# Optimization experiments

Measured on AMD Instinct MI355X. Metric: run time of the kernel, lower is better.

## Reference

```python
import jax, jax.numpy as jnp
import numpy as np

B, N, DIM = 16, 4096, 256
EXP = 4
COV_EPS = 1e-08


def setup_inputs() -> dict:
    key = jax.random.key(0)
    ks = jax.random.split(key, 9)
    s = 1.0 / np.sqrt(DIM)
    sh = 1.0 / np.sqrt(DIM * EXP)
    return {
        "x": jax.random.normal(ks[0], (B, N, DIM), dtype=jnp.float32),
        # IsoFFN: Linear(dim, 4*dim) -> GELU -> Linear(4*dim, dim) + residual (dropout inactive at eval)
        "W1": jax.random.uniform(ks[1], (DIM, DIM * EXP), minval=-s, maxval=s, dtype=jnp.float32),
        "b1": jnp.zeros((DIM * EXP,), jnp.float32),
        "W2": jax.random.uniform(ks[2], (DIM * EXP, DIM), minval=-sh, maxval=sh, dtype=jnp.float32),
        "b2": jnp.zeros((DIM,), jnp.float32),
        # eigenvalue head: Linear(dim, 3) + Softplus
        "Wval": jax.random.uniform(ks[3], (DIM, 3), minval=-s, maxval=s, dtype=jnp.float32),
        "bval": jnp.zeros((3,), jnp.float32),
        # eigenvector head: Linear(dim, 9)
        "Wvec": jax.random.uniform(ks[4], (DIM, 9), minval=-s, maxval=s, dtype=jnp.float32),
        "bvec": jnp.zeros((9,), jnp.float32),
    }


def reference(x, W1, b1, W2, b2, Wval, bval, Wvec, bvec):
    b, n, c = x.shape
    # IsoFFN (eval mode: dropout = identity), residual connection
    h = x + jax.nn.gelu(x @ W1 + b1) @ W2 + b2
    # eigenvalue head -> positive eigenvalues -> diagonal [B*N, 3, 3]
    eigvals = jax.nn.softplus(h @ Wval + bval).reshape(b * n, 3)
    L = jnp.zeros((b * n, 3, 3), h.dtype).at[:, jnp.arange(3), jnp.arange(3)].set(eigvals)
    # eigenvector head -> batched tiny QR to orthonormalize
    V = (h @ Wvec + bvec).reshape(b * n, 3, 3)
    Q, _ = jnp.linalg.qr(V)  # batched 3x3 QR
    # cov = Q L Q^T
    cov = jnp.einsum('bij,bjk,blk->bil', Q, L, Q).reshape(b, n, 3, 3)
    cov = (cov + jnp.swapaxes(cov, -2, -1)) * 0.5
    cov = cov + COV_EPS * jnp.eye(3, dtype=cov.dtype)
    return cov
```

## Files before the change

### kernel.cpp

```cpp
#include <hip/hip_runtime.h>
#include <cstdint>
#include <cstddef>

#define TOKENS   65536
#define KDIM     256
#define HIDDEN   1024
#define BM       128
#define HC       32
#define NCHUNK   32
#define NTHREADS 512
#define NBLOCKS  (TOKENS / BM)

#define GOFF  131072
#define B1OFF 147456
#define LDS_BYTES 151552

using f16x8 = __attribute__((ext_vector_type(8))) _Float16;
using f16x4 = __attribute__((ext_vector_type(4))) _Float16;
using f32x4 = __attribute__((ext_vector_type(4))) float;
using u32x4 = __attribute__((ext_vector_type(4))) uint32_t;

__device__ __align__(16) _Float16 g_W1h[NCHUNK * HC * KDIM];
__device__ __align__(16) _Float16 g_W1l[NCHUNK * HC * KDIM];
__device__ __align__(16) _Float16 g_W2h[NCHUNK * KDIM * HC];
__device__ __align__(16) _Float16 g_W2l[NCHUNK * KDIM * HC];
__device__ __align__(16) _Float16 g_Whh[16 * KDIM];
__device__ __align__(16) _Float16 g_Whl[16 * KDIM];

__global__ __launch_bounds__(256) void prep_kernel(
    const float* __restrict__ W1, const float* __restrict__ W2,
    const float* __restrict__ Wval, const float* __restrict__ Wvec) {
  const int tid = blockIdx.x * 256 + threadIdx.x;
  if (tid < 32768) {
    const int c = tid >> 10, n = (tid >> 5) & 31, gd = tid & 31;
    const int g = gd ^ (n & 7);
    const int hid = c * 32 + n;
    f16x8 hv, lv;
#pragma unroll
    for (int j = 0; j < 8; ++j) {
      const float wv = W1[(g * 8 + j) * HIDDEN + hid];
      const _Float16 hi = (_Float16)wv;
      hv[j] = hi;
      lv[j] = (_Float16)(wv - (float)hi);
    }
    const int dst = c * 8192 + n * 256 + gd * 8;
    *(f16x8*)(g_W1h + dst) = hv;
    *(f16x8*)(g_W1l + dst) = lv;
  } else if (tid < 65536) {
    const int t = tid - 32768;
    const int c = t >> 10, n = (t >> 2) & 255, gd = t & 3;
    const int g = gd ^ ((n >> 1) & 3);
    f16x8 hv, lv;
#pragma unroll
    for (int j = 0; j < 8; ++j) {
      const float wv = W2[(c * 32 + g * 8 + j) * KDIM + n];
      const _Float16 hi = (_Float16)wv;
      hv[j] = hi;
      lv[j] = (_Float16)(wv - (float)hi);
    }
    const int dst = c * 8192 + n * 32 + gd * 8;
    *(f16x8*)(g_W2h + dst) = hv;
    *(f16x8*)(g_W2l + dst) = lv;
  } else if (tid < 65536 + 4096) {
    const int e = tid - 65536;
    const int j16 = e >> 8, k = e & 255;
    float wv = 0.f;
    if (j16 < 3) wv = Wval[k * 3 + j16];
    else if (j16 < 12) wv = Wvec[k * 9 + (j16 - 3)];
    const _Float16 hi = (_Float16)wv;
    g_Whh[e] = hi;
    g_Whl[e] = (_Float16)(wv - (float)hi);
  }
}

__device__ __forceinline__ void stage_chunk(char* buf, int c, int w, int lane) {
  const int plane = w >> 1, half = w & 1;
  const _Float16* g;
  if      (plane == 0) g = g_W1h;
  else if (plane == 1) g = g_W1l;
  else if (plane == 2) g = g_W2h;
  else                 g = g_W2l;
  const char* s = (const char*)g + (size_t)c * 16384 + half * 8192 + lane * 16;
  char* d = buf + plane * 16384 + half * 8192;
#pragma unroll
  for (int i = 0; i < 8; ++i) {
    __builtin_amdgcn_global_load_lds(
        (__attribute__((address_space(1))) void*)(void*)(s + i * 1024),
        (__attribute__((address_space(3))) void*)(d + i * 1024), 16, 0, 0);
  }
}

__device__ __forceinline__ f16x8 unpack_half(const u32x4 a, const u32x4 b, uint32_t sel) {
  u32x4 r;
  r[0] = __builtin_amdgcn_perm(a[1], a[0], sel);
  r[1] = __builtin_amdgcn_perm(a[3], a[2], sel);
  r[2] = __builtin_amdgcn_perm(b[1], b[0], sel);
  r[3] = __builtin_amdgcn_perm(b[3], b[2], sel);
  return __builtin_bit_cast(f16x8, r);
}

__global__ __launch_bounds__(NTHREADS, 2) void fused_kernel(
    const float* __restrict__ x, const float* __restrict__ b1,
    const float* __restrict__ b2, const float* __restrict__ bval,
    const float* __restrict__ bvec, float* __restrict__ out) {
  extern __shared__ char smem[];
  const int tid  = threadIdx.x;
  const int lane = tid & 63;
  const int w    = tid >> 6;
  const int wm   = w >> 1;
  const int wn   = w & 1;
  const int l15  = lane & 15;
  const int lg   = lane >> 4;
  const int64_t R = (int64_t)blockIdx.x * BM;

  {
    float* b1l = (float*)(smem + B1OFF);
    b1l[tid]       = b1[tid];
    b1l[tid + 512] = b1[tid + 512];
  }

  {
    const float* xg = x + R * KDIM;
#pragma unroll
    for (int i = 0; i < 16; ++i) {
      const int fidx = tid + NTHREADS * i;
      const int row  = fidx >> 6;
      const int f4   = fidx & 63;
      const float4 v = *(const float4*)(xg + row * KDIM + f4 * 4);
      const _Float16 h0 = (_Float16)v.x, h1 = (_Float16)v.y,
                     h2 = (_Float16)v.z, h3 = (_Float16)v.w;
      f16x4 hv = {h0, h1, h2, h3};
      f16x4 lv = {(_Float16)(v.x - (float)h0), (_Float16)(v.y - (float)h1),
                  (_Float16)(v.z - (float)h2), (_Float16)(v.w - (float)h3)};
      const uint32_t off = (uint32_t)(row * 512) +
                           (((uint32_t)(f4 * 8)) ^ ((row & 7) << 4));
      *(f16x4*)(smem + off)         = hv;
      *(f16x4*)(smem + 65536 + off) = lv;
    }
  }
  __syncthreads();

  f16x8 xah[2][8], xal[2][8];
#pragma unroll
  for (int mt = 0; mt < 2; ++mt) {
    const int row = wm * 32 + mt * 16 + l15;
    const uint32_t rbase = row * 512;
    const uint32_t swz = (row & 7) << 4;
#pragma unroll
    for (int ks = 0; ks < 8; ++ks) {
      const uint32_t off = rbase + (((uint32_t)((ks * 32 + lg * 8) * 2)) ^ swz);
      xah[mt][ks] = *(const f16x8*)(smem + off);
      xal[mt][ks] = *(const f16x8*)(smem + 65536 + off);
    }
  }
  asm volatile("s_waitcnt lgkmcnt(0)" ::: "memory");
  __builtin_amdgcn_s_barrier();
  __builtin_amdgcn_sched_barrier(0);

  stage_chunk(smem,         0, w, lane);
  stage_chunk(smem + 65536, 1, w, lane);

  const f32x4 z4 = {0.f, 0.f, 0.f, 0.f};
  f32x4 acc2[2][8];
#pragma unroll
  for (int mt = 0; mt < 2; ++mt)
#pragma unroll
    for (int nt = 0; nt < 8; ++nt) acc2[mt][nt] = z4;

#pragma unroll 1
  for (int t = 0; t < NCHUNK; ++t) {
    char* buf = smem + ((t & 1) ? 65536 : 0);
    if (t == NCHUNK - 1) { asm volatile("s_waitcnt vmcnt(0)" ::: "memory"); }
    else                 { asm volatile("s_waitcnt vmcnt(8)" ::: "memory"); }
    __builtin_amdgcn_s_barrier();
    __builtin_amdgcn_sched_barrier(0);

    f32x4 accA[2] = {z4, z4}, accB[2] = {z4, z4}, accC[2] = {z4, z4};
    {
      const int n = wn * 16 + l15;
      const uint32_t nbase = (uint32_t)(n * 512);
      const uint32_t nswz  = (uint32_t)((n & 7) << 4);
#pragma unroll
      for (int ks = 0; ks < 8; ++ks) {
        const uint32_t off = nbase + (((uint32_t)(ks * 64 + lg * 16)) ^ nswz);
        const f16x8 bh = *(const f16x8*)(buf + off);
        const f16x8 bl = *(const f16x8*)(buf + 16384 + off);
#pragma unroll
        for (int mt = 0; mt < 2; ++mt) {
          accA[mt] = __builtin_amdgcn_mfma_f32_16x16x32_f16(xah[mt][ks], bh, accA[mt], 0, 0, 0);
          accB[mt] = __builtin_amdgcn_mfma_f32_16x16x32_f16(xah[mt][ks], bl, accB[mt], 0, 0, 0);
          accC[mt] = __builtin_amdgcn_mfma_f32_16x16x32_f16(xal[mt][ks], bh, accC[mt], 0, 0, 0);
        }
      }
    }

    {
      const float bv = ((const float*)(smem + B1OFF))[t * 32 + wn * 16 + l15];
      const int gcol = wn * 16 + l15;
#pragma unroll
      for (int mt = 0; mt < 2; ++mt) {
#pragma unroll
        for (int r = 0; r < 4; ++r) {
          const float v  = accA[mt][r] + accB[mt][r] + accC[mt][r] + bv;
          const float u  = 0.79788456080286535588f * (v + 0.044715f * v * v * v);
          const float e  = __expf(2.f * u);
          const float th = 1.f - 2.f / (e + 1.f);
          const float gv = 0.5f * v * (1.f + th);
          const _Float16 gh = (_Float16)gv;
          const _Float16 gl = (_Float16)(gv - (float)gh);
          const uint32_t pk = (uint32_t)__builtin_bit_cast(unsigned short, gh) |
                              ((uint32_t)__builtin_bit_cast(unsigned short, gl) << 16);
          const int grow = wm * 32 + mt * 16 + lg * 4 + r;
          const uint32_t off = (uint32_t)(GOFF + grow * 128) +
                               (((uint32_t)(gcol * 4)) ^ ((grow & 7) << 4));
          *(uint32_t*)(smem + off) = pk;
        }
      }
    }
    asm volatile("s_waitcnt lgkmcnt(0)" ::: "memory");
    __builtin_amdgcn_s_barrier();
    __builtin_amdgcn_sched_barrier(0);

    {
      f16x8 ah[2], al[2];
#pragma unroll
      for (int mt = 0; mt < 2; ++mt) {
        const int row = wm * 32 + mt * 16 + l15;
        const uint32_t sw = (uint32_t)((row & 7) << 4);
        const uint32_t base = (uint32_t)(GOFF + row * 128);
        const u32x4 w0 = *(const u32x4*)(smem + base + (((uint32_t)(lg * 32)) ^ sw));
        const u32x4 w1 = *(const u32x4*)(smem + base + (((uint32_t)(lg * 32 + 16)) ^ sw));
        ah[mt] = unpack_half(w0, w1, 0x05040100u);
        al[mt] = unpack_half(w0, w1, 0x07060302u);
      }
#pragma unroll
      for (int nt = 0; nt < 8; ++nt) {
        const int n = wn * 128 + nt * 16 + l15;
        const uint32_t off = (uint32_t)(n * 64) +
                             (((uint32_t)(lg * 16)) ^ (((n >> 1) & 3) << 4));
        const f16x8 bh = *(const f16x8*)(buf + 32768 + off);
        const f16x8 bl = *(const f16x8*)(buf + 49152 + off);
#pragma unroll
        for (int mt = 0; mt < 2; ++mt) {
          acc2[mt][nt] = __builtin_amdgcn_mfma_f32_16x16x32_f16(ah[mt], bh, acc2[mt][nt], 0, 0, 0);
          acc2[mt][nt] = __builtin_amdgcn_mfma_f32_16x16x32_f16(ah[mt], bl, acc2[mt][nt], 0, 0, 0);
          acc2[mt][nt] = __builtin_amdgcn_mfma_f32_16x16x32_f16(al[mt], bh, acc2[mt][nt], 0, 0, 0);
        }
      }
    }
    __builtin_amdgcn_sched_barrier(0);
    __builtin_amdgcn_s_barrier();
    __builtin_amdgcn_sched_barrier(0);
    if (t + 2 < NCHUNK) stage_chunk(buf, t + 2, w, lane);
  }

  {
    const float* xg = x + R * KDIM;
#pragma unroll
    for (int nt = 0; nt < 8; ++nt) {
      const float bv = b2[wn * 128 + nt * 16 + l15];
#pragma unroll
      for (int mt = 0; mt < 2; ++mt) {
#pragma unroll
        for (int r = 0; r < 4; ++r) {
          const int row = wm * 32 + mt * 16 + lg * 4 + r;
          const int col = wn * 128 + nt * 16 + l15;
          const float h = acc2[mt][nt][r] + xg[row * KDIM + col] + bv;
          acc2[mt][nt][r] = h;
          const uint32_t off = (uint32_t)(row * 512) +
                               (((uint32_t)(col * 2)) ^ ((row & 7) << 4));
          *(_Float16*)(smem + off) = (_Float16)h;
        }
      }
    }
  }
  __syncthreads();

  f32x4 hacc = z4;
  const int hrow = wm * 32 + wn * 16 + l15;
  const uint32_t hbase = hrow * 512;
  const uint32_t hswz  = (hrow & 7) << 4;
#pragma unroll
  for (int ks = 0; ks < 8; ++ks) {
    const uint32_t off = hbase + (((uint32_t)((ks * 32 + lg * 8) * 2)) ^ hswz);
    const f16x8 af  = *(const f16x8*)(smem + off);
    const f16x8 bhf = *(const f16x8*)(g_Whh + l15 * 256 + ks * 32 + lg * 8);
    const f16x8 blf = *(const f16x8*)(g_Whl + l15 * 256 + ks * 32 + lg * 8);
    hacc = __builtin_amdgcn_mfma_f32_16x16x32_f16(af, bhf, hacc, 0, 0, 0);
    hacc = __builtin_amdgcn_mfma_f32_16x16x32_f16(af, blf, hacc, 0, 0, 0);
  }
  __syncthreads();

#pragma unroll
  for (int nt = 0; nt < 8; ++nt) {
#pragma unroll
    for (int mt = 0; mt < 2; ++mt) {
#pragma unroll
      for (int r = 0; r < 4; ++r) {
        const int row = wm * 32 + mt * 16 + lg * 4 + r;
        const int col = wn * 128 + nt * 16 + l15;
        const float h = acc2[mt][nt][r];
        const _Float16 hh = (_Float16)h;
        const uint32_t off = (uint32_t)(row * 512) +
                             (((uint32_t)(col * 2)) ^ ((row & 7) << 4));
        *(_Float16*)(smem + off) = (_Float16)(h - (float)hh);
      }
    }
  }
  __syncthreads();

#pragma unroll
  for (int ks = 0; ks < 8; ++ks) {
    const uint32_t off = hbase + (((uint32_t)((ks * 32 + lg * 8) * 2)) ^ hswz);
    const f16x8 af  = *(const f16x8*)(smem + off);
    const f16x8 bhf = *(const f16x8*)(g_Whh + l15 * 256 + ks * 32 + lg * 8);
    hacc = __builtin_amdgcn_mfma_f32_16x16x32_f16(af, bhf, hacc, 0, 0, 0);
  }
  const float hb = (l15 < 3) ? bval[l15] : ((l15 < 12) ? bvec[l15 - 3] : 0.f);
#pragma unroll
  for (int r = 0; r < 4; ++r) hacc[r] += hb;

  float* hstg = (float*)(smem + 65536);
#pragma unroll
  for (int r = 0; r < 4; ++r) {
    const int row = wm * 32 + wn * 16 + lg * 4 + r;
    hstg[row * 16 + l15] = hacc[r];
  }
  if (lane < 16) {
    const int row = wm * 32 + wn * 16 + lane;
    const float* hs = hstg + row * 16;
    float sp[3];
#pragma unroll
    for (int i = 0; i < 3; ++i) {
      const float s = hs[i];
      sp[i] = fmaxf(s, 0.f) + log1pf(__expf(-fabsf(s)));
    }
    const float a0 = hs[3], a1 = hs[6], a2 = hs[9];
    const float b0 = hs[4], bc1 = hs[7], bc2 = hs[10];
    const float na = a0 * a0 + a1 * a1 + a2 * a2;
    const float ia = 1.f / sqrtf(fmaxf(na, 1e-30f));
    const float q00 = a0 * ia, q01 = a1 * ia, q02 = a2 * ia;
    const float d  = q00 * b0 + q01 * bc1 + q02 * bc2;
    const float u0 = b0 - d * q00, u1 = bc1 - d * q01, u2 = bc2 - d * q02;
    const float nu = u0 * u0 + u1 * u1 + u2 * u2;
    const float iu = 1.f / sqrtf(fmaxf(nu, 1e-30f));
    const float q10 = u0 * iu, q11 = u1 * iu, q12 = u2 * iu;
    const float q20 = q01 * q12 - q02 * q11;
    const float q21 = q02 * q10 - q00 * q12;
    const float q22 = q00 * q11 - q01 * q10;
    const float c00 = sp[0]*q00*q00 + sp[1]*q10*q10 + sp[2]*q20*q20 + 1e-8f;
    const float c11 = sp[0]*q01*q01 + sp[1]*q11*q11 + sp[2]*q21*q21 + 1e-8f;
    const float c22 = sp[0]*q02*q02 + sp[1]*q12*q12 + sp[2]*q22*q22 + 1e-8f;
    const float c01 = sp[0]*q00*q01 + sp[1]*q10*q11 + sp[2]*q20*q21;
    const float c02 = sp[0]*q00*q02 + sp[1]*q10*q12 + sp[2]*q20*q22;
    const float c12 = sp[0]*q01*q02 + sp[1]*q11*q12 + sp[2]*q21*q22;
    float* o = out + (size_t)(R + row) * 9;
    o[0] = c00; o[1] = c01; o[2] = c02;
    o[3] = c01; o[4] = c11; o[5] = c12;
    o[6] = c02; o[7] = c12; o[8] = c22;
  }
}

extern "C" void kernel_launch(void* const* d_in, const int* in_sizes, int n_in,
                              void* d_out, int out_size, void* d_ws, size_t ws_size,
                              hipStream_t stream) {
  const float* x    = (const float*)d_in[0];
  const float* W1   = (const float*)d_in[1];
  const float* b1   = (const float*)d_in[2];
  const float* W2   = (const float*)d_in[3];
  const float* b2   = (const float*)d_in[4];
  const float* Wval = (const float*)d_in[5];
  const float* bval = (const float*)d_in[6];
  const float* Wvec = (const float*)d_in[7];
  const float* bvec = (const float*)d_in[8];
  float* out = (float*)d_out;
  (void)in_sizes; (void)n_in; (void)out_size; (void)d_ws; (void)ws_size;

  hipFuncSetAttribute((const void*)fused_kernel,
                      hipFuncAttributeMaxDynamicSharedMemorySize, LDS_BYTES);

  prep_kernel<<<272, 256, 0, stream>>>(W1, W2, Wval, Wvec);
  fused_kernel<<<NBLOCKS, NTHREADS, LDS_BYTES, stream>>>(x, b1, b2, bval, bvec, out);
}
```

Baseline: 287.6 us.

## Software-pipeline GEMM1 and GEMM2 across chunks with double-buffered GELU tiles

Restructures the chunk loop so GEMM1 for chunk T runs in the same phase as GEMM2 for chunk T-1, using double-buffered G tiles and separate W1/W2 staging buffers. This cuts the number of barriers per chunk from three to two and lets the MFMA work from both GEMMs interleave. It also merges two correction accumulators into one, simplifies the GELU into a single exp and fast divide, and loads b1 from global memory one chunk ahead instead of staging it in LDS. LDS use grows to 160KB, and the changed staging order and barrier scheme could introduce hazards.

Result: slower. 384.1 us (+33.6%).

```diff
diff --git a/kernel.cpp b/kernel.cpp
--- a/kernel.cpp
+++ b/kernel.cpp
@@ -11,9 +11,9 @@
 #define NTHREADS 512
 #define NBLOCKS  (TOKENS / BM)
 
+#define W2OFF 65536
 #define GOFF  131072
-#define B1OFF 147456
-#define LDS_BYTES 151552
+#define LDS_BYTES 163840
 
 using f16x8 = __attribute__((ext_vector_type(8))) _Float16;
 using f16x4 = __attribute__((ext_vector_type(4))) _Float16;
@@ -73,17 +73,23 @@
   }
 }
 
-__device__ __forceinline__ void stage_chunk(char* buf, int c, int w, int lane) {
-  const int plane = w >> 1, half = w & 1;
-  const _Float16* g;
-  if      (plane == 0) g = g_W1h;
-  else if (plane == 1) g = g_W1l;
-  else if (plane == 2) g = g_W2h;
-  else                 g = g_W2l;
-  const char* s = (const char*)g + (size_t)c * 16384 + half * 8192 + lane * 16;
-  char* d = buf + plane * 16384 + half * 8192;
-#pragma unroll
-  for (int i = 0; i < 8; ++i) {
+__device__ __forceinline__ void stage_W1(char* smem, int par, int c, int w, int lane) {
+  const char* base = (w < 4) ? (const char*)g_W1h : (const char*)g_W1l;
+  const char* s = base + (size_t)c * 16384 + (size_t)(w & 3) * 4096 + (size_t)lane * 16;
+  char* d = smem + par * 32768 + ((w < 4) ? 0 : 16384) + (w & 3) * 4096;
+#pragma unroll
+  for (int i = 0; i < 4; ++i) {
+    __builtin_amdgcn_global_load_lds(
+        (__attribute__((address_space(1))) void*)(void*)(s + i * 1024),
+        (__attribute__((address_space(3))) void*)(d + i * 1024), 16, 0, 0);
+  }
+}
+__device__ __forceinline__ void stage_W2(char* smem, int par, int c, int w, int lane) {
+  const char* base = (w < 4) ? (const char*)g_W2h : (const char*)g_W2l;
+  const char* s = base + (size_t)c * 16384 + (size_t)(w & 3) * 4096 + (size_t)lane * 16;
+  char* d = smem + W2OFF + par * 32768 + ((w < 4) ? 0 : 16384) + (w & 3) * 4096;
+#pragma unroll
+  for (int i = 0; i < 4; ++i) {
     __builtin_amdgcn_global_load_lds(
         (__attribute__((address_space(1))) void*)(void*)(s + i * 1024),
         (__attribute__((address_space(3))) void*)(d + i * 1024), 16, 0, 0);
@@ -97,6 +103,114 @@
   r[2] = __builtin_amdgcn_perm(b[1], b[0], sel);
   r[3] = __builtin_amdgcn_perm(b[3], b[2], sel);
   return __builtin_bit_cast(f16x8, r);
+}
+
+#define MFMA16(a, b, c) __builtin_amdgcn_mfma_f32_16x16x32_f16((a), (b), (c), 0, 0, 0)
+
+template <int PAR, bool DO_G2>
+__device__ __forceinline__ void chunk_body(
+    int T, char* __restrict__ smem,
+    const f16x8 (&xah)[2][8], const f16x8 (&xal)[2][8],
+    f32x4 (&acc2)[2][8], float& b_cur, const float* __restrict__ b1g,
+    int wm, int wn, int l15, int lg, int w, int lane) {
+  const f32x4 z4 = {0.f, 0.f, 0.f, 0.f};
+
+  float b_nxt = 0.f;
+  if (T < 32) {
+    int idx = (T + 1) * 32 + wn * 16 + l15;
+    idx = idx > 1023 ? 1023 : idx;
+    b_nxt = b1g[idx];
+  }
+
+  f32x4 accA[2] = {z4, z4}, accB[2] = {z4, z4};
+  if (T < 32) {
+    const int n = wn * 16 + l15;
+    const uint32_t nbase = (uint32_t)(n * 512);
+    const uint32_t nswz  = (uint32_t)((n & 7) << 4);
+    const char* w1b = smem + PAR * 32768;
+#pragma unroll
+    for (int ks = 0; ks < 8; ++ks) {
+      const uint32_t off = nbase + (((uint32_t)(ks * 64 + lg * 16)) ^ nswz);
+      const f16x8 bh = *(const f16x8*)(w1b + off);
+      const f16x8 bl = *(const f16x8*)(w1b + 16384 + off);
+#pragma unroll
+      for (int mt = 0; mt < 2; ++mt) {
+        accA[mt] = MFMA16(xah[mt][ks], bh, accA[mt]);
+        accB[mt] = MFMA16(xah[mt][ks], bl, accB[mt]);
+        accB[mt] = MFMA16(xal[mt][ks], bh, accB[mt]);
+      }
+    }
+  }
+
+  if (DO_G2) {
+    const char* w2b = smem + W2OFF + (PAR ^ 1) * 32768;
+    const char* gb  = smem + GOFF + (PAR ^ 1) * 16384;
+    f16x8 ah[2], al[2];
+#pragma unroll
+    for (int mt = 0; mt < 2; ++mt) {
+      const int row = wm * 32 + mt * 16 + l15;
+      const uint32_t sw = (uint32_t)((row & 7) << 4);
+      const uint32_t base = (uint32_t)(row * 128);
+      const u32x4 w0 = *(const u32x4*)(gb + base + (((uint32_t)(lg * 32)) ^ sw));
+      const u32x4 w1v = *(const u32x4*)(gb + base + (((uint32_t)(lg * 32 + 16)) ^ sw));
+      ah[mt] = unpack_half(w0, w1v, 0x05040100u);
+      al[mt] = unpack_half(w0, w1v, 0x07060302u);
+    }
+#pragma unroll
+    for (int nt = 0; nt < 8; ++nt) {
+      const int n = wn * 128 + nt * 16 + l15;
+      const uint32_t off = (uint32_t)(n * 64) +
+                           (((uint32_t)(lg * 16)) ^ (((n >> 1) & 3) << 4));
+      const f16x8 bh = *(const f16x8*)(w2b + off);
+      const f16x8 bl = *(const f16x8*)(w2b + 16384 + off);
+#pragma unroll
+      for (int mt = 0; mt < 2; ++mt) {
+        acc2[mt][nt] = MFMA16(ah[mt], bh, acc2[mt][nt]);
+        acc2[mt][nt] = MFMA16(ah[mt], bl, acc2[mt][nt]);
+        acc2[mt][nt] = MFMA16(al[mt], bh, acc2[mt][nt]);
+      }
+    }
+  }
+
+  if (T < 32) {
+    constexpr float C2 = -1.5957691216057308f;
+    constexpr float A2 = -0.071355071222456f;
+    const int gcol = wn * 16 + l15;
+    char* gw = smem + GOFF + PAR * 16384;
+#pragma unroll
+    for (int mt = 0; mt < 2; ++mt) {
+#pragma unroll
+      for (int r = 0; r < 4; ++r) {
+        const float v  = accA[mt][r] + accB[mt][r] + b_cur;
+        const float v2 = v * v;
+        const float tE = v * __builtin_fmaf(v2, A2, C2);
+        const float e  = __expf(tE);
+        const float gv = __fdividef(v, 1.f + e);
+        const _Float16 gh = (_Float16)gv;
+        const _Float16 gl = (_Float16)(gv - (float)gh);
+        const uint32_t pk = (uint32_t)__builtin_bit_cast(unsigned short, gh) |
+                            ((uint32_t)__builtin_bit_cast(unsigned short, gl) << 16);
+        const int grow = wm * 32 + mt * 16 + lg * 4 + r;
+        const uint32_t off = (uint32_t)(grow * 128) +
+                             (((uint32_t)(gcol * 4)) ^ ((grow & 7) << 4));
+        *(uint32_t*)(gw + off) = pk;
+      }
+    }
+  }
+  b_cur = b_nxt;
+
+  asm volatile("s_waitcnt lgkmcnt(0)" ::: "memory");
+  __builtin_amdgcn_s_barrier();
+  __builtin_amdgcn_sched_barrier(0);
+
+  if (T < 32) {
+    stage_W1(smem, PAR, (T + 2 > 31) ? T : T + 2, w, lane);
+    stage_W2(smem, PAR ^ 1, (T + 1 > 31) ? 30 : T + 1, w, lane);
+  }
+
+  asm volatile("s_waitcnt vmcnt(8)" ::: "memory");
+  __builtin_amdgcn_s_barrier();
+  __builtin_amdgcn_sched_barrier(0);
 }
 
 __global__ __launch_bounds__(NTHREADS, 2) void fused_kernel(
@@ -112,12 +226,6 @@
   const int l15  = lane & 15;
   const int lg   = lane >> 4;
   const int64_t R = (int64_t)blockIdx.x * BM;
-
-  {
-    float* b1l = (float*)(smem + B1OFF);
-    b1l[tid]       = b1[tid];
-    b1l[tid + 512] = b1[tid + 512];
-  }
 
   {
     const float* xg = x + R * KDIM;
@@ -153,13 +261,17 @@
       xal[mt][ks] = *(const f16x8*)(smem + 65536 + off);
     }
   }
-  asm volatile("s_waitcnt lgkmcnt(0)" ::: "memory");
+  __syncthreads();
+
+  float b_cur = b1[wn * 16 + l15];
+  asm volatile("s_waitcnt vmcnt(0)" ::: "memory");
+  stage_W1(smem, 0, 0, w, lane);
+  stage_W2(smem, 0, 0, w, lane);
+  stage_W1(smem, 1, 1, w, lane);
+  asm volatile("s_waitcnt vmcnt(8)" ::: "memory");
   __builtin_amdgcn_s_barrier();
   __builtin_amdgcn_sched_barrier(0);
 
-  stage_chunk(smem,         0, w, lane);
-  stage_chunk(smem + 65536, 1, w, lane);
-
   const f32x4 z4 = {0.f, 0.f, 0.f, 0.f};
   f32x4 acc2[2][8];
 #pragma unroll
@@ -167,92 +279,13 @@
 #pragma unroll
     for (int nt = 0; nt < 8; ++nt) acc2[mt][nt] = z4;
 
+  chunk_body<0, false>(0, smem, xah, xal, acc2, b_cur, b1, wm, wn, l15, lg, w, lane);
 #pragma unroll 1
-  for (int t = 0; t < NCHUNK; ++t) {
-    char* buf = smem + ((t & 1) ? 65536 : 0);
-    if (t == NCHUNK - 1) { asm volatile("s_waitcnt vmcnt(0)" ::: "memory"); }
-    else                 { asm volatile("s_waitcnt vmcnt(8)" ::: "memory"); }
-    __builtin_amdgcn_s_barrier();
-    __builtin_amdgcn_sched_barrier(0);
-
-    f32x4 accA[2] = {z4, z4}, accB[2] = {z4, z4}, accC[2] = {z4, z4};
-    {
-      const int n = wn * 16 + l15;
-      const uint32_t nbase = (uint32_t)(n * 512);
-      const uint32_t nswz  = (uint32_t)((n & 7) << 4);
-#pragma unroll
-      for (int ks = 0; ks < 8; ++ks) {
-        const uint32_t off = nbase + (((uint32_t)(ks * 64 + lg * 16)) ^ nswz);
-        const f16x8 bh = *(const f16x8*)(buf + off);
-        const f16x8 bl = *(const f16x8*)(buf + 16384 + off);
-#pragma unroll
-        for (int mt = 0; mt < 2; ++mt) {
-          accA[mt] = __builtin_amdgcn_mfma_f32_16x16x32_f16(xah[mt][ks], bh, accA[mt], 0, 0, 0);
-          accB[mt] = __builtin_amdgcn_mfma_f32_16x16x32_f16(xah[mt][ks], bl, accB[mt], 0, 0, 0);
-          accC[mt] = __builtin_amdgcn_mfma_f32_16x16x32_f16(xal[mt][ks], bh, accC[mt], 0, 0, 0);
-        }
-      }
-    }
-
-    {
-      const float bv = ((const float*)(smem + B1OFF))[t * 32 + wn * 16 + l15];
-      const int gcol = wn * 16 + l15;
-#pragma unroll
-      for (int mt = 0; mt < 2; ++mt) {
-#pragma unroll
-        for (int r = 0; r < 4; ++r) {
-          const float v  = accA[mt][r] + accB[mt][r] + accC[mt][r] + bv;
-          const float u  = 0.79788456080286535588f * (v + 0.044715f * v * v * v);
-          const float e  = __expf(2.f * u);
-          const float th = 1.f - 2.f / (e + 1.f);
-          const float gv = 0.5f * v * (1.f + th);
-          const _Float16 gh = (_Float16)gv;
-          const _Float16 gl = (_Float16)(gv - (float)gh);
-          const uint32_t pk = (uint32_t)__builtin_bit_cast(unsigned short, gh) |
-                              ((uint32_t)__builtin_bit_cast(unsigned short, gl) << 16);
-          const int grow = wm * 32 + mt * 16 + lg * 4 + r;
-          const uint32_t off = (uint32_t)(GOFF + grow * 128) +
-                               (((uint32_t)(gcol * 4)) ^ ((grow & 7) << 4));
-          *(uint32_t*)(smem + off) = pk;
-        }
-      }
-    }
-    asm volatile("s_waitcnt lgkmcnt(0)" ::: "memory");
-    __builtin_amdgcn_s_barrier();
-    __builtin_amdgcn_sched_barrier(0);
-
-    {
-      f16x8 ah[2], al[2];
-#pragma unroll
-      for (int mt = 0; mt < 2; ++mt) {
-        const int row = wm * 32 + mt * 16 + l15;
-        const uint32_t sw = (uint32_t)((row & 7) << 4);
-        const uint32_t base = (uint32_t)(GOFF + row * 128);
-        const u32x4 w0 = *(const u32x4*)(smem + base + (((uint32_t)(lg * 32)) ^ sw));
-        const u32x4 w1 = *(const u32x4*)(smem + base + (((uint32_t)(lg * 32 + 16)) ^ sw));
-        ah[mt] = unpack_half(w0, w1, 0x05040100u);
-        al[mt] = unpack_half(w0, w1, 0x07060302u);
-      }
-#pragma unroll
-      for (int nt = 0; nt < 8; ++nt) {
-        const int n = wn * 128 + nt * 16 + l15;
-        const uint32_t off = (uint32_t)(n * 64) +
-                             (((uint32_t)(lg * 16)) ^ (((n >> 1) & 3) << 4));
-        const f16x8 bh = *(const f16x8*)(buf + 32768 + off);
-        const f16x8 bl = *(const f16x8*)(buf + 49152 + off);
-#pragma unroll
-        for (int mt = 0; mt < 2; ++mt) {
-          acc2[mt][nt] = __builtin_amdgcn_mfma_f32_16x16x32_f16(ah[mt], bh, acc2[mt][nt], 0, 0, 0);
-          acc2[mt][nt] = __builtin_amdgcn_mfma_f32_16x16x32_f16(ah[mt], bl, acc2[mt][nt], 0, 0, 0);
-          acc2[mt][nt] = __builtin_amdgcn_mfma_f32_16x16x32_f16(al[mt], bh, acc2[mt][nt], 0, 0, 0);
-        }
-      }
-    }
-    __builtin_amdgcn_sched_barrier(0);
-    __builtin_amdgcn_s_barrier();
-    __builtin_amdgcn_sched_barrier(0);
-    if (t + 2 < NCHUNK) stage_chunk(buf, t + 2, w, lane);
-  }
+  for (int tt = 0; tt < 16; ++tt) {
+    chunk_body<1, true>(2 * tt + 1, smem, xah, xal, acc2, b_cur, b1, wm, wn, l15, lg, w, lane);
+    chunk_body<0, true>(2 * tt + 2, smem, xah, xal, acc2, b_cur, b1, wm, wn, l15, lg, w, lane);
+  }
+  __syncthreads();
 
   {
     const float* xg = x + R * KDIM;
@@ -286,8 +319,8 @@
     const f16x8 af  = *(const f16x8*)(smem + off);
     const f16x8 bhf = *(const f16x8*)(g_Whh + l15 * 256 + ks * 32 + lg * 8);
     const f16x8 blf = *(const f16x8*)(g_Whl + l15 * 256 + ks * 32 + lg * 8);
-    hacc = __builtin_amdgcn_mfma_f32_16x16x32_f16(af, bhf, hacc, 0, 0, 0);
-    hacc = __builtin_amdgcn_mfma_f32_16x16x32_f16(af, blf, hacc, 0, 0, 0);
+    hacc = MFMA16(af, bhf, hacc);
+    hacc = MFMA16(af, blf, hacc);
   }
   __syncthreads();
 
@@ -314,7 +347,7 @@
     const uint32_t off = hbase + (((uint32_t)((ks * 32 + lg * 8) * 2)) ^ hswz);
     const f16x8 af  = *(const f16x8*)(smem + off);
     const f16x8 bhf = *(const f16x8*)(g_Whh + l15 * 256 + ks * 32 + lg * 8);
-    hacc = __builtin_amdgcn_mfma_f32_16x16x32_f16(af, bhf, hacc, 0, 0, 0);
+    hacc = MFMA16(af, bhf, hacc);
   }
   const float hb = (l15 < 3) ? bval[l15] : ((l15 < 12) ? bvec[l15 - 3] : 0.f);
 #pragma unroll
```
